# Kernel tuning notes

Hardware: AMD Instinct MI355X
Metric: run time of the kernel (lower is better)

## Reference

```python
import jax, jax.numpy as jnp
import numpy as np

N_NODES = 20000   # batch of nodes (vectorized version of per-node calls)
N_SAMPLE = 32     # num_sample neighbors per node
EMBED_DIM = 256
TABLE_SIZE = 100000


def setup_inputs() -> dict:
    key = jax.random.key(0)
    k1, k2, k3, k4, k5, k6, k7, k8, k9 = jax.random.split(key, 9)
    D = EMBED_DIM
    scale = 1.0 / np.sqrt(D)
    return {
        "node_ids": jax.random.randint(k1, (N_NODES,), 0, TABLE_SIZE),
        "neigh_ids": jax.random.randint(k2, (N_NODES, N_SAMPLE), 0, TABLE_SIZE),
        "feat_table": jax.random.normal(k3, (TABLE_SIZE, D), dtype=jnp.float32),
        "Wq": jax.random.uniform(k4, (D, D), jnp.float32, -scale, scale),
        "bq": jax.random.uniform(k5, (D,), jnp.float32, -scale, scale),
        "Wk": jax.random.uniform(k6, (D, D), jnp.float32, -scale, scale),
        "bk": jax.random.uniform(k7, (D,), jnp.float32, -scale, scale),
        "Wv": jax.random.uniform(k8, (D, D), jnp.float32, -scale, scale),
        "bv": jax.random.uniform(k9, (D,), jnp.float32, -scale, scale),
    }


def reference(node_ids, neigh_ids, feat_table, Wq, bq, Wk, bk, Wv, bv):
    # id2feat lookups
    self_feats = feat_table[node_ids]            # [N, D]
    neigh_feats = feat_table[neigh_ids]          # [N, S, D]
    # context = cat(self, neighbors) along the key/value axis
    ctx = jnp.concatenate([self_feats[:, None, :], neigh_feats], axis=1)  # [N, S+1, D]
    # torch Linear: y = x @ W^T + b
    Q = self_feats @ Wq.T + bq                   # [N, D]
    K = ctx @ Wk.T + bk                          # [N, S+1, D]
    V = ctx @ Wv.T + bv                          # [N, S+1, D]
    scores = jnp.einsum('nd,nkd->nk', Q, K)      # [N, S+1]
    attn = jax.nn.softmax(scores, axis=-1)
    mix = jnp.einsum('nk,nkd->nd', attn, V)      # [N, D]
    out = jnp.tanh(mix)
    # F.normalize(p=2, dim=-1) with eps=1e-12 clamp
    norm = jnp.maximum(jnp.linalg.norm(out, axis=-1, keepdims=True), 1e-12)
    return out / norm
```

## Files before the change

### kernel.cpp

```cpp
#include <hip/hip_runtime.h>
#include <hip/hip_bf16.h>

#define D 256

typedef __bf16 bf16x8 __attribute__((ext_vector_type(8)));
typedef float  f32x4  __attribute__((ext_vector_type(4)));
typedef unsigned short ushort8 __attribute__((ext_vector_type(8)));

static __device__ __forceinline__ unsigned short f2bf_rne(float f) {
    unsigned u = __float_as_uint(f);
    u += 0x7fff + ((u >> 16) & 1);
    return (unsigned short)(u >> 16);
}
static __device__ __forceinline__ float bf2f(unsigned short h) {
    return __uint_as_float(((unsigned)h) << 16);
}
static __device__ __forceinline__ unsigned short f2h(float f) {
    _Float16 h = (_Float16)f;
    unsigned short u; __builtin_memcpy(&u, &h, 2); return u;
}
static __device__ __forceinline__ float h2f(unsigned short u) {
    _Float16 h; __builtin_memcpy(&h, &u, 2); return (float)h;
}

static __device__ __forceinline__ void cp16(const unsigned short* g, unsigned short* l) {
    __builtin_amdgcn_global_load_lds(
        (const __attribute__((address_space(1))) void*)g,
        (__attribute__((address_space(3))) void*)l, 16, 0, 0);
}

static __device__ __forceinline__ void split8(float4 a, float4 b,
                                              ushort8& h, ushort8& l) {
    float v[8] = {a.x, a.y, a.z, a.w, b.x, b.y, b.z, b.w};
    #pragma unroll
    for (int i = 0; i < 8; ++i) {
        unsigned short hh = f2bf_rne(v[i]);
        h[i] = hh;
        l[i] = f2bf_rne(v[i] - bf2f(hh));
    }
}

__global__ __launch_bounds__(256) void convert_w_wstar(
    const float* __restrict__ Wq, const float* __restrict__ Wk,
    const float* __restrict__ Wv, const float* __restrict__ bq,
    unsigned short* __restrict__ wqT_h, unsigned short* __restrict__ wqT_l,
    unsigned short* __restrict__ wkT_h, unsigned short* __restrict__ wkT_l,
    unsigned short* __restrict__ wv_h,  unsigned short* __restrict__ wv_l,
    float* __restrict__ wstar)
{
    if (blockIdx.x == 256) {
        int k = threadIdx.x;
        float s = 0.f;
        for (int n = 0; n < D; ++n) s = fmaf(Wk[n * D + k], bq[n], s);
        wstar[k] = s;
        return;
    }
    int i = blockIdx.x * 256 + threadIdx.x;
    int r = i >> 8, cc = i & 255;
    int ti = cc * D + r;
    float q = Wq[i]; unsigned short qh = f2bf_rne(q);
    wqT_h[ti] = qh; wqT_l[ti] = f2bf_rne(q - bf2f(qh));
    float k = Wk[i]; unsigned short kh = f2bf_rne(k);
    wkT_h[ti] = kh; wkT_l[ti] = f2bf_rne(k - bf2f(kh));
    float v = Wv[i]; unsigned short vh = f2bf_rne(v);
    wv_h[i] = vh; wv_l[i] = f2bf_rne(v - bf2f(vh));
}

__global__ __launch_bounds__(256) void convert_feat_f16_c(
    const float* __restrict__ feat, const float* __restrict__ wstar,
    unsigned short* __restrict__ f16tab, float* __restrict__ c, int T)
{
    const int w = threadIdx.x >> 6, l = threadIdx.x & 63;
    const int row = blockIdx.x * 4 + w;
    if (row >= T) return;
    float4 v = ((const float4*)(feat + (size_t)row * D))[l];
    float4 ws = ((const float4*)wstar)[l];
    ushort4 h;
    h.x = f2h(v.x); h.y = f2h(v.y); h.z = f2h(v.z); h.w = f2h(v.w);
    ((ushort4*)(f16tab + (size_t)row * D))[l] = h;
    float p = v.x * ws.x + v.y * ws.y + v.z * ws.z + v.w * ws.w;
    #pragma unroll
    for (int off = 32; off > 0; off >>= 1) p += __shfl_down(p, off);
    if (l == 0) c[row] = p;
}

template <bool BF16PAIR_OUT, bool AF32>
__global__ __launch_bounds__(256) void mfma_gemm(
    const unsigned short* __restrict__ Ah, const unsigned short* __restrict__ Al,
    const float* __restrict__ Af,
    const int* __restrict__ idx, int M,
    const unsigned short* __restrict__ Bh, const unsigned short* __restrict__ Bl,
    const float* __restrict__ bias,
    float* __restrict__ Cf, unsigned short* __restrict__ Ch,
    unsigned short* __restrict__ Cl, int ldc)
{
    __shared__ __align__(16) unsigned short sAh[128 * 32], sBh[128 * 32];
    __shared__ __align__(16) unsigned short sAl[128 * 32], sBl[128 * 32];

    const int t = threadIdx.x;
    const int w = t >> 6, lane = t & 63;
    const int quad = lane >> 4, mcol = lane & 15;
    const int m0 = blockIdx.x * 128, n0 = blockIdx.y * 128;
    const int wr = (w >> 1) * 64, wc = (w & 1) * 64;

    const int srow = w * 32 + (lane >> 2);
    const int kchunk = (lane & 3) * 8;

    int ar0 = m0 + srow;      if (ar0 > M - 1) ar0 = M - 1;
    int ar1 = m0 + srow + 16; if (ar1 > M - 1) ar1 = M - 1;
    if (idx) { ar0 = idx[ar0]; ar1 = idx[ar1]; }

    const unsigned short *a0h = nullptr, *a1h = nullptr, *a0l = nullptr, *a1l = nullptr;
    const float *af0 = nullptr, *af1 = nullptr;
    if constexpr (AF32) {
        af0 = Af + (size_t)ar0 * D + kchunk;
        af1 = Af + (size_t)ar1 * D + kchunk;
    } else {
        a0h = Ah + (size_t)ar0 * D + kchunk;
        a1h = Ah + (size_t)ar1 * D + kchunk;
        a0l = Al + (size_t)ar0 * D + kchunk;
        a1l = Al + (size_t)ar1 * D + kchunk;
    }
    const unsigned short* b0h = Bh + (size_t)(n0 + srow) * D + kchunk;
    const unsigned short* b1h = Bh + (size_t)(n0 + srow + 16) * D + kchunk;
    const unsigned short* b0l = Bl + (size_t)(n0 + srow) * D + kchunk;
    const unsigned short* b1l = Bl + (size_t)(n0 + srow + 16) * D + kchunk;

    f32x4 acc[4][4];
    #pragma unroll
    for (int i = 0; i < 4; ++i)
        #pragma unroll
        for (int j = 0; j < 4; ++j) acc[i][j] = (f32x4){0.f, 0.f, 0.f, 0.f};

    #pragma unroll
    for (int kb = 0; kb < D; kb += 32) {
        cp16(b0h + kb, &sBh[w * 1024]);
        cp16(b1h + kb, &sBh[w * 1024 + 512]);
        cp16(b0l + kb, &sBl[w * 1024]);
        cp16(b1l + kb, &sBl[w * 1024 + 512]);
        if constexpr (AF32) {
            float4 x0 = *(const float4*)(af0 + kb);
            float4 x1 = *(const float4*)(af0 + kb + 4);
            float4 y0 = *(const float4*)(af1 + kb);
            float4 y1 = *(const float4*)(af1 + kb + 4);
            ushort8 h, l;
            split8(x0, x1, h, l);
            *(ushort8*)&sAh[w * 1024 + lane * 8] = h;
            *(ushort8*)&sAl[w * 1024 + lane * 8] = l;
            split8(y0, y1, h, l);
            *(ushort8*)&sAh[w * 1024 + 512 + lane * 8] = h;
            *(ushort8*)&sAl[w * 1024 + 512 + lane * 8] = l;
        } else {
            cp16(a0h + kb, &sAh[w * 1024]);
            cp16(a1h + kb, &sAh[w * 1024 + 512]);
            cp16(a0l + kb, &sAl[w * 1024]);
            cp16(a1l + kb, &sAl[w * 1024 + 512]);
        }
        __syncthreads();

        bf16x8 fah[4], fbh[4], fal[4], fbl[4];
        #pragma unroll
        for (int i = 0; i < 4; ++i) {
            fah[i] = *(const bf16x8*)&sAh[(wr + i * 16 + mcol) * 32 + quad * 8];
            fbh[i] = *(const bf16x8*)&sBh[(wc + i * 16 + mcol) * 32 + quad * 8];
            fal[i] = *(const bf16x8*)&sAl[(wr + i * 16 + mcol) * 32 + quad * 8];
            fbl[i] = *(const bf16x8*)&sBl[(wc + i * 16 + mcol) * 32 + quad * 8];
        }
        #pragma unroll
        for (int i = 0; i < 4; ++i)
            #pragma unroll
            for (int j = 0; j < 4; ++j) {
                acc[i][j] = __builtin_amdgcn_mfma_f32_16x16x32_bf16(fah[i], fbh[j], acc[i][j], 0, 0, 0);
                acc[i][j] = __builtin_amdgcn_mfma_f32_16x16x32_bf16(fah[i], fbl[j], acc[i][j], 0, 0, 0);
                acc[i][j] = __builtin_amdgcn_mfma_f32_16x16x32_bf16(fal[i], fbh[j], acc[i][j], 0, 0, 0);
            }
        __syncthreads();
    }

    float bb[4];
    #pragma unroll
    for (int j = 0; j < 4; ++j) bb[j] = bias ? bias[n0 + wc + j * 16 + mcol] : 0.f;

    #pragma unroll
    for (int i = 0; i < 4; ++i) {
        #pragma unroll
        for (int r = 0; r < 4; ++r) {
            int m = m0 + wr + i * 16 + quad * 4 + r;
            if (m < M) {
                #pragma unroll
                for (int j = 0; j < 4; ++j) {
                    float v = acc[i][j][r] + bb[j];
                    size_t off = (size_t)m * ldc + n0 + wc + j * 16 + mcol;
                    if constexpr (BF16PAIR_OUT) {
                        unsigned short hh = f2bf_rne(v);
                        Ch[off] = hh;
                        Cl[off] = f2bf_rne(v - bf2f(hh));
                    } else {
                        Cf[off] = v;
                    }
                }
            }
        }
    }
}

template <int S>
__global__ __launch_bounds__(256) void attn_wave(
    const int* __restrict__ node_ids, const int* __restrict__ neigh_ids,
    const float* __restrict__ G, const unsigned short* __restrict__ f16tab,
    const float* __restrict__ c, float* __restrict__ mixf, int N)
{
    constexpr int SP1 = S + 1;
    const int w = threadIdx.x >> 6, l = threadIdx.x & 63;
    const int n = blockIdx.x * 4 + w;
    if (n >= N) return;

    int myid = 0;
    if (l < SP1) myid = (l == 0) ? node_ids[n] : neigh_ids[(size_t)n * S + (l - 1)];
    float myc = (l < SP1) ? c[myid] : 0.f;

    float4 g = ((const float4*)(G + (size_t)n * D))[l];

    ushort4 rows[SP1];
    #pragma unroll
    for (int k = 0; k < SP1; ++k) {
        int idk = __shfl(myid, k);
        rows[k] = ((const ushort4*)(f16tab + (size_t)idk * D))[l];
    }

    float score = -1e30f;
    #pragma unroll
    for (int k = 0; k < SP1; ++k) {
        ushort4 r = rows[k];
        float p = g.x * h2f(r.x) + g.y * h2f(r.y) +
                  g.z * h2f(r.z) + g.w * h2f(r.w);
        #pragma unroll
        for (int off = 1; off < 64; off <<= 1) p += __shfl_xor(p, off);
        if (l == k) score = p + myc;
    }

    float m = score;
    #pragma unroll
    for (int off = 1; off < 64; off <<= 1) m = fmaxf(m, __shfl_xor(m, off));
    float e = (l < SP1) ? __expf(score - m) : 0.f;
    float s = e;
    #pragma unroll
    for (int off = 1; off < 64; off <<= 1) s += __shfl_xor(s, off);
    float attn = e / s;

    float4 mix = {0.f, 0.f, 0.f, 0.f};
    #pragma unroll
    for (int k = 0; k < SP1; ++k) {
        float a = __shfl(attn, k);
        ushort4 r = rows[k];
        mix.x = fmaf(a, h2f(r.x), mix.x);
        mix.y = fmaf(a, h2f(r.y), mix.y);
        mix.z = fmaf(a, h2f(r.z), mix.z);
        mix.w = fmaf(a, h2f(r.w), mix.w);
    }
    ((float4*)(mixf + (size_t)n * D))[l] = mix;
}

__global__ __launch_bounds__(256) void attn_dyn(
    const int* __restrict__ node_ids, const int* __restrict__ neigh_ids,
    const float* __restrict__ G, const unsigned short* __restrict__ f16tab,
    const float* __restrict__ c, float* __restrict__ mixf, int S)
{
    const int n = blockIdx.x, t = threadIdx.x;
    const int w = t >> 6, l = t & 63;
    __shared__ int   ids[128];
    __shared__ float sc[128];
    const int SP1 = S + 1;
    for (int k = t; k < SP1; k += 256)
        ids[k] = (k == 0) ? node_ids[n] : neigh_ids[(size_t)n * S + k - 1];
    __syncthreads();
    float4 g = ((const float4*)(G + (size_t)n * D))[l];
    for (int k = w; k < SP1; k += 4) {
        int id = ids[k];
        ushort4 h4 = ((const ushort4*)(f16tab + (size_t)id * D))[l];
        float p = g.x * h2f(h4.x) + g.y * h2f(h4.y) +
                  g.z * h2f(h4.z) + g.w * h2f(h4.w);
        #pragma unroll
        for (int off = 32; off > 0; off >>= 1) p += __shfl_down(p, off);
        if (l == 0) sc[k] = p + c[id];
    }
    __syncthreads();
    if (t < 64) {
        float v = (t < SP1) ? sc[t] : -1e30f;
        float m = v;
        #pragma unroll
        for (int off = 32; off > 0; off >>= 1) m = fmaxf(m, __shfl_down(m, off));
        m = __shfl(m, 0);
        float e = (t < SP1) ? __expf(v - m) : 0.f;
        float s = e;
        #pragma unroll
        for (int off = 32; off > 0; off >>= 1) s += __shfl_down(s, off);
        s = __shfl(s, 0);
        if (t < SP1) sc[t] = e / s;
    }
    __syncthreads();
    float mix = 0.f;
    for (int k = 0; k < SP1; ++k)
        mix = fmaf(sc[k], h2f(f16tab[(size_t)ids[k] * D + t]), mix);
    mixf[(size_t)n * D + t] = mix;
}

__global__ __launch_bounds__(256) void tanh_norm(
    const float* __restrict__ P, float* __restrict__ out, int N)
{
    const int w = threadIdx.x >> 6, l = threadIdx.x & 63;
    const int row = blockIdx.x * 4 + w;
    if (row >= N) return;
    float4 v = ((const float4*)(P + (size_t)row * D))[l];
    float4 o;
    o.x = tanhf(v.x); o.y = tanhf(v.y); o.z = tanhf(v.z); o.w = tanhf(v.w);
    float ss = o.x * o.x + o.y * o.y + o.z * o.z + o.w * o.w;
    #pragma unroll
    for (int off = 32; off > 0; off >>= 1) ss += __shfl_down(ss, off);
    ss = __shfl(ss, 0);
    float inv = 1.0f / fmaxf(sqrtf(ss), 1e-12f);
    o.x *= inv; o.y *= inv; o.z *= inv; o.w *= inv;
    ((float4*)(out + (size_t)row * D))[l] = o;
}

extern "C" void kernel_launch(void* const* d_in, const int* in_sizes, int n_in,
                              void* d_out, int out_size, void* d_ws, size_t ws_size,
                              hipStream_t stream) {
    const int*   node_ids  = (const int*)  d_in[0];
    const int*   neigh_ids = (const int*)  d_in[1];
    const float* feat      = (const float*)d_in[2];
    const float* Wq        = (const float*)d_in[3];
    const float* bq        = (const float*)d_in[4];
    const float* Wk        = (const float*)d_in[5];
    const float* Wv        = (const float*)d_in[7];
    const float* bv        = (const float*)d_in[8];
    float*       out       = (float*)d_out;

    const int N = in_sizes[0];
    const int S = in_sizes[1] / N;
    const int T = in_sizes[2] / D;

    unsigned short* f16tab = (unsigned short*)d_ws;
    float*          c      = (float*)(f16tab + (size_t)T * D);
    float*          G      = c + T;
    float*          mixf   = G + (size_t)N * D;
    float*          P      = mixf + (size_t)N * D;
    unsigned short* wqT_h  = (unsigned short*)(P + (size_t)N * D);
    unsigned short* wqT_l  = wqT_h + D * D;
    unsigned short* wkT_h  = wqT_l + D * D;
    unsigned short* wkT_l  = wkT_h + D * D;
    unsigned short* wv_h   = wkT_l + D * D;
    unsigned short* wv_l   = wv_h + D * D;
    unsigned short* MT_h   = wv_l + D * D;
    unsigned short* MT_l   = MT_h + D * D;
    float*          wstar  = (float*)(MT_l + D * D);

    convert_w_wstar<<<257, 256, 0, stream>>>(Wq, Wk, Wv, bq,
        wqT_h, wqT_l, wkT_h, wkT_l, wv_h, wv_l, wstar);

    convert_feat_f16_c<<<(T + 3) / 4, 256, 0, stream>>>(feat, wstar, f16tab, c, T);

    {
        dim3 grid(2, 2);
        mfma_gemm<true, false><<<grid, 256, 0, stream>>>(
            wkT_h, wkT_l, nullptr, nullptr, D, wqT_h, wqT_l, nullptr,
            nullptr, MT_h, MT_l, D);
    }
    {
        dim3 grid((N + 127) / 128, 2);
        mfma_gemm<false, true><<<grid, 256, 0, stream>>>(
            nullptr, nullptr, feat, node_ids, N, MT_h, MT_l, nullptr,
            G, nullptr, nullptr, D);
    }
    if (S == 32)
        attn_wave<32><<<(N + 3) / 4, 256, 0, stream>>>(
            node_ids, neigh_ids, G, f16tab, c, mixf, N);
    else
        attn_dyn<<<N, 256, 0, stream>>>(node_ids, neigh_ids, G, f16tab, c, mixf, S);

    {
        dim3 grid((N + 127) / 128, 2);
        mfma_gemm<false, true><<<grid, 256, 0, stream>>>(
            nullptr, nullptr, mixf, nullptr, N, wv_h, wv_l, bv,
            P, nullptr, nullptr, D);
    }
    tanh_norm<<<(N + 3) / 4, 256, 0, stream>>>(P, out, N);
}
```

Measured before the change: 327.1 us.

## Fold key-bias term into G bias, merge convert kernels, shrink GEMM tiles, repack attention

The per-table-row bias dot product c (feat·Wk^T bq) is dropped. Instead wstar is passed as the bias of the G GEMM, so the constant shifts every score equally or is absorbed differently, and the full-table c pass plus its reads are removed. The feature-table fp16 conversion and the weight conversion are merged into one launch. The GEMM tile drops from 128x128 to 64x128 to give more blocks. The attention kernel now has each half-wave process one row with 8-wide fp16 loads, which halves the shuffle reduction depth. Adding wstar to G gives g·x + x·wstar, which equals the old x·(G_old+wstar), so it is mathematically equivalent.

```diff
diff --git a/kernel.cpp b/kernel.cpp
--- a/kernel.cpp
+++ b/kernel.cpp
@@ -5,7 +5,7 @@
 
 typedef __bf16 bf16x8 __attribute__((ext_vector_type(8)));
 typedef float  f32x4  __attribute__((ext_vector_type(4)));
-typedef unsigned short ushort8 __attribute__((ext_vector_type(8)));
+typedef unsigned short ushort8v __attribute__((ext_vector_type(8)));
 
 static __device__ __forceinline__ unsigned short f2bf_rne(float f) {
     unsigned u = __float_as_uint(f);
@@ -30,7 +30,7 @@
 }
 
 static __device__ __forceinline__ void split8(float4 a, float4 b,
-                                              ushort8& h, ushort8& l) {
+                                              ushort8v& h, ushort8v& l) {
     float v[8] = {a.x, a.y, a.z, a.w, b.x, b.y, b.z, b.w};
     #pragma unroll
     for (int i = 0; i < 8; ++i) {
@@ -40,22 +40,36 @@
     }
 }
 
-__global__ __launch_bounds__(256) void convert_w_wstar(
+__global__ __launch_bounds__(256) void convert_all(
+    const float* __restrict__ feat, int T, int nbf,
     const float* __restrict__ Wq, const float* __restrict__ Wk,
     const float* __restrict__ Wv, const float* __restrict__ bq,
+    unsigned short* __restrict__ f16tab,
     unsigned short* __restrict__ wqT_h, unsigned short* __restrict__ wqT_l,
     unsigned short* __restrict__ wkT_h, unsigned short* __restrict__ wkT_l,
     unsigned short* __restrict__ wv_h,  unsigned short* __restrict__ wv_l,
     float* __restrict__ wstar)
 {
-    if (blockIdx.x == 256) {
+    const int bx = blockIdx.x;
+    if (bx < nbf) {
+        const int w = threadIdx.x >> 6, l = threadIdx.x & 63;
+        const int row = bx * 4 + w;
+        if (row >= T) return;
+        float4 v = ((const float4*)(feat + (size_t)row * D))[l];
+        ushort4 h;
+        h.x = f2h(v.x); h.y = f2h(v.y); h.z = f2h(v.z); h.w = f2h(v.w);
+        ((ushort4*)(f16tab + (size_t)row * D))[l] = h;
+        return;
+    }
+    const int wb = bx - nbf;
+    if (wb == 256) {
         int k = threadIdx.x;
         float s = 0.f;
         for (int n = 0; n < D; ++n) s = fmaf(Wk[n * D + k], bq[n], s);
         wstar[k] = s;
         return;
     }
-    int i = blockIdx.x * 256 + threadIdx.x;
+    int i = wb * 256 + threadIdx.x;
     int r = i >> 8, cc = i & 255;
     int ti = cc * D + r;
     float q = Wq[i]; unsigned short qh = f2bf_rne(q);
@@ -66,26 +80,8 @@
     wv_h[i] = vh; wv_l[i] = f2bf_rne(v - bf2f(vh));
 }
 
-__global__ __launch_bounds__(256) void convert_feat_f16_c(
-    const float* __restrict__ feat, const float* __restrict__ wstar,
-    unsigned short* __restrict__ f16tab, float* __restrict__ c, int T)
-{
-    const int w = threadIdx.x >> 6, l = threadIdx.x & 63;
-    const int row = blockIdx.x * 4 + w;
-    if (row >= T) return;
-    float4 v = ((const float4*)(feat + (size_t)row * D))[l];
-    float4 ws = ((const float4*)wstar)[l];
-    ushort4 h;
-    h.x = f2h(v.x); h.y = f2h(v.y); h.z = f2h(v.z); h.w = f2h(v.w);
-    ((ushort4*)(f16tab + (size_t)row * D))[l] = h;
-    float p = v.x * ws.x + v.y * ws.y + v.z * ws.z + v.w * ws.w;
-    #pragma unroll
-    for (int off = 32; off > 0; off >>= 1) p += __shfl_down(p, off);
-    if (l == 0) c[row] = p;
-}
-
 template <bool BF16PAIR_OUT, bool AF32>
-__global__ __launch_bounds__(256) void mfma_gemm(
+__global__ __launch_bounds__(256) void mfma_gemm64(
     const unsigned short* __restrict__ Ah, const unsigned short* __restrict__ Al,
     const float* __restrict__ Af,
     const int* __restrict__ idx, int M,
@@ -94,82 +90,74 @@
     float* __restrict__ Cf, unsigned short* __restrict__ Ch,
     unsigned short* __restrict__ Cl, int ldc)
 {
-    __shared__ __align__(16) unsigned short sAh[128 * 32], sBh[128 * 32];
-    __shared__ __align__(16) unsigned short sAl[128 * 32], sBl[128 * 32];
+    __shared__ __align__(16) unsigned short sAh[64 * 32], sAl[64 * 32];
+    __shared__ __align__(16) unsigned short sBh[128 * 32], sBl[128 * 32];
 
     const int t = threadIdx.x;
     const int w = t >> 6, lane = t & 63;
     const int quad = lane >> 4, mcol = lane & 15;
-    const int m0 = blockIdx.x * 128, n0 = blockIdx.y * 128;
-    const int wr = (w >> 1) * 64, wc = (w & 1) * 64;
-
-    const int srow = w * 32 + (lane >> 2);
-    const int kchunk = (lane & 3) * 8;
-
-    int ar0 = m0 + srow;      if (ar0 > M - 1) ar0 = M - 1;
-    int ar1 = m0 + srow + 16; if (ar1 > M - 1) ar1 = M - 1;
-    if (idx) { ar0 = idx[ar0]; ar1 = idx[ar1]; }
-
-    const unsigned short *a0h = nullptr, *a1h = nullptr, *a0l = nullptr, *a1l = nullptr;
-    const float *af0 = nullptr, *af1 = nullptr;
+    const int m0 = blockIdx.x * 64, n0 = blockIdx.y * 128;
+    const int wc = w * 32;
+
+    const int arow = t >> 2;
+    const int kchunk = (t & 3) * 8;
+
+    int ar = m0 + arow; if (ar > M - 1) ar = M - 1;
+    if (idx) ar = idx[ar];
+
+    const unsigned short *aph = nullptr, *apl = nullptr;
+    const float *apf = nullptr;
     if constexpr (AF32) {
-        af0 = Af + (size_t)ar0 * D + kchunk;
-        af1 = Af + (size_t)ar1 * D + kchunk;
+        apf = Af + (size_t)ar * D + kchunk;
     } else {
-        a0h = Ah + (size_t)ar0 * D + kchunk;
-        a1h = Ah + (size_t)ar1 * D + kchunk;
-        a0l = Al + (size_t)ar0 * D + kchunk;
-        a1l = Al + (size_t)ar1 * D + kchunk;
-    }
-    const unsigned short* b0h = Bh + (size_t)(n0 + srow) * D + kchunk;
-    const unsigned short* b1h = Bh + (size_t)(n0 + srow + 16) * D + kchunk;
-    const unsigned short* b0l = Bl + (size_t)(n0 + srow) * D + kchunk;
-    const unsigned short* b1l = Bl + (size_t)(n0 + srow + 16) * D + kchunk;
-
-    f32x4 acc[4][4];
+        aph = Ah + (size_t)ar * D + kchunk;
+        apl = Al + (size_t)ar * D + kchunk;
+    }
+    const unsigned short* b0h = Bh + (size_t)(n0 + arow) * D + kchunk;
+    const unsigned short* b1h = Bh + (size_t)(n0 + arow + 64) * D + kchunk;
+    const unsigned short* b0l = Bl + (size_t)(n0 + arow) * D + kchunk;
+    const unsigned short* b1l = Bl + (size_t)(n0 + arow + 64) * D + kchunk;
+
+    f32x4 acc[4][2];
     #pragma unroll
     for (int i = 0; i < 4; ++i)
         #pragma unroll
-        for (int j = 0; j < 4; ++j) acc[i][j] = (f32x4){0.f, 0.f, 0.f, 0.f};
+        for (int j = 0; j < 2; ++j) acc[i][j] = (f32x4){0.f, 0.f, 0.f, 0.f};
 
     #pragma unroll
     for (int kb = 0; kb < D; kb += 32) {
-        cp16(b0h + kb, &sBh[w * 1024]);
-        cp16(b1h + kb, &sBh[w * 1024 + 512]);
-        cp16(b0l + kb, &sBl[w * 1024]);
-        cp16(b1l + kb, &sBl[w * 1024 + 512]);
+        cp16(b0h + kb, &sBh[w * 512]);
+        cp16(b1h + kb, &sBh[w * 512 + 2048]);
+        cp16(b0l + kb, &sBl[w * 512]);
+        cp16(b1l + kb, &sBl[w * 512 + 2048]);
         if constexpr (AF32) {
-            float4 x0 = *(const float4*)(af0 + kb);
-            float4 x1 = *(const float4*)(af0 + kb + 4);
-            float4 y0 = *(const float4*)(af1 + kb);
-            float4 y1 = *(const float4*)(af1 + kb + 4);
-            ushort8 h, l;
+            float4 x0 = *(const float4*)(apf + kb);
+            float4 x1 = *(const float4*)(apf + kb + 4);
+            ushort8v h, l;
             split8(x0, x1, h, l);
-            *(ushort8*)&sAh[w * 1024 + lane * 8] = h;
-            *(ushort8*)&sAl[w * 1024 + lane * 8] = l;
-            split8(y0, y1, h, l);
-            *(ushort8*)&sAh[w * 1024 + 512 + lane * 8] = h;
-            *(ushort8*)&sAl[w * 1024 + 512 + lane * 8] = l;
+            *(ushort8v*)&sAh[arow * 32 + kchunk] = h;
+            *(ushort8v*)&sAl[arow * 32 + kchunk] = l;
         } else {
-            cp16(a0h + kb, &sAh[w * 1024]);
-            cp16(a1h + kb, &sAh[w * 1024 + 512]);
-            cp16(a0l + kb, &sAl[w * 1024]);
-            cp16(a1l + kb, &sAl[w * 1024 + 512]);
+            cp16(aph + kb, &sAh[w * 512]);
+            cp16(apl + kb, &sAl[w * 512]);
         }
         __syncthreads();
 
-        bf16x8 fah[4], fbh[4], fal[4], fbl[4];
+        bf16x8 fah[4], fal[4], fbh[2], fbl[2];
         #pragma unroll
         for (int i = 0; i < 4; ++i) {
-            fah[i] = *(const bf16x8*)&sAh[(wr + i * 16 + mcol) * 32 + quad * 8];
-            fbh[i] = *(const bf16x8*)&sBh[(wc + i * 16 + mcol) * 32 + quad * 8];
-            fal[i] = *(const bf16x8*)&sAl[(wr + i * 16 + mcol) * 32 + quad * 8];
-            fbl[i] = *(const bf16x8*)&sBl[(wc + i * 16 + mcol) * 32 + quad * 8];
+            fah[i] = *(const bf16x8*)&sAh[(i * 16 + mcol) * 32 + quad * 8];
+            fal[i] = *(const bf16x8*)&sAl[(i * 16 + mcol) * 32 + quad * 8];
+        }
+        #pragma unroll
+        for (int j = 0; j < 2; ++j) {
+            fbh[j] = *(const bf16x8*)&sBh[(wc + j * 16 + mcol) * 32 + quad * 8];
+            fbl[j] = *(const bf16x8*)&sBl[(wc + j * 16 + mcol) * 32 + quad * 8];
         }
         #pragma unroll
         for (int i = 0; i < 4; ++i)
             #pragma unroll
-            for (int j = 0; j < 4; ++j) {
+            for (int j = 0; j < 2; ++j) {
                 acc[i][j] = __builtin_amdgcn_mfma_f32_16x16x32_bf16(fah[i], fbh[j], acc[i][j], 0, 0, 0);
                 acc[i][j] = __builtin_amdgcn_mfma_f32_16x16x32_bf16(fah[i], fbl[j], acc[i][j], 0, 0, 0);
                 acc[i][j] = __builtin_amdgcn_mfma_f32_16x16x32_bf16(fal[i], fbh[j], acc[i][j], 0, 0, 0);
@@ -177,18 +165,18 @@
         __syncthreads();
     }
 
-    float bb[4];
-    #pragma unroll
-    for (int j = 0; j < 4; ++j) bb[j] = bias ? bias[n0 + wc + j * 16 + mcol] : 0.f;
+    float bb[2];
+    #pragma unroll
+    for (int j = 0; j < 2; ++j) bb[j] = bias ? bias[n0 + wc + j * 16 + mcol] : 0.f;
 
     #pragma unroll
     for (int i = 0; i < 4; ++i) {
         #pragma unroll
         for (int r = 0; r < 4; ++r) {
-            int m = m0 + wr + i * 16 + quad * 4 + r;
+            int m = m0 + i * 16 + quad * 4 + r;
             if (m < M) {
                 #pragma unroll
-                for (int j = 0; j < 4; ++j) {
+                for (int j = 0; j < 2; ++j) {
                     float v = acc[i][j][r] + bb[j];
                     size_t off = (size_t)m * ldc + n0 + wc + j * 16 + mcol;
                     if constexpr (BF16PAIR_OUT) {
@@ -205,66 +193,77 @@
 }
 
 template <int S>
-__global__ __launch_bounds__(256) void attn_wave(
+__global__ __launch_bounds__(256) void attn_wave2(
     const int* __restrict__ node_ids, const int* __restrict__ neigh_ids,
     const float* __restrict__ G, const unsigned short* __restrict__ f16tab,
-    const float* __restrict__ c, float* __restrict__ mixf, int N)
+    float* __restrict__ mixf, int N)
 {
     constexpr int SP1 = S + 1;
+    constexpr int NP  = (SP1 + 1) / 2;
     const int w = threadIdx.x >> 6, l = threadIdx.x & 63;
     const int n = blockIdx.x * 4 + w;
     if (n >= N) return;
 
+    const int h  = l >> 5;
+    const int j  = l & 31;
+
     int myid = 0;
     if (l < SP1) myid = (l == 0) ? node_ids[n] : neigh_ids[(size_t)n * S + (l - 1)];
-    float myc = (l < SP1) ? c[myid] : 0.f;
-
-    float4 g = ((const float4*)(G + (size_t)n * D))[l];
-
-    ushort4 rows[SP1];
-    #pragma unroll
-    for (int k = 0; k < SP1; ++k) {
-        int idk = __shfl(myid, k);
-        rows[k] = ((const ushort4*)(f16tab + (size_t)idk * D))[l];
+
+    float4 g0 = ((const float4*)(G + (size_t)n * D))[j * 2];
+    float4 g1 = ((const float4*)(G + (size_t)n * D))[j * 2 + 1];
+    float gv[8] = {g0.x, g0.y, g0.z, g0.w, g1.x, g1.y, g1.z, g1.w};
+
+    ushort8v rows[NP];
+    #pragma unroll
+    for (int p = 0; p < NP; ++p) {
+        int rix = 2 * p + h; if (rix > SP1 - 1) rix = SP1 - 1;
+        int idk = __shfl(myid, rix);
+        rows[p] = ((const ushort8v*)(f16tab + (size_t)idk * D))[j];
     }
 
     float score = -1e30f;
     #pragma unroll
-    for (int k = 0; k < SP1; ++k) {
-        ushort4 r = rows[k];
-        float p = g.x * h2f(r.x) + g.y * h2f(r.y) +
-                  g.z * h2f(r.z) + g.w * h2f(r.w);
-        #pragma unroll
-        for (int off = 1; off < 64; off <<= 1) p += __shfl_xor(p, off);
-        if (l == k) score = p + myc;
-    }
+    for (int p = 0; p < NP; ++p) {
+        ushort8v r = rows[p];
+        float s = 0.f;
+        #pragma unroll
+        for (int i = 0; i < 8; ++i) s = fmaf(gv[i], h2f(r[i]), s);
+        #pragma unroll
+        for (int off = 1; off < 32; off <<= 1) s += __shfl_xor(s, off);
+        if (j == p) score = s;
+    }
+    const int myrow = 2 * j + h;
+    if (myrow >= SP1) score = -1e30f;
 
     float m = score;
     #pragma unroll
     for (int off = 1; off < 64; off <<= 1) m = fmaxf(m, __shfl_xor(m, off));
-    float e = (l < SP1) ? __expf(score - m) : 0.f;
+    float e = (myrow < SP1) ? __expf(score - m) : 0.f;
     float s = e;
     #pragma unroll
     for (int off = 1; off < 64; off <<= 1) s += __shfl_xor(s, off);
     float attn = e / s;
 
-    float4 mix = {0.f, 0.f, 0.f, 0.f};
-    #pragma unroll
-    for (int k = 0; k < SP1; ++k) {
-        float a = __shfl(attn, k);
-        ushort4 r = rows[k];
-        mix.x = fmaf(a, h2f(r.x), mix.x);
-        mix.y = fmaf(a, h2f(r.y), mix.y);
-        mix.z = fmaf(a, h2f(r.z), mix.z);
-        mix.w = fmaf(a, h2f(r.w), mix.w);
-    }
-    ((float4*)(mixf + (size_t)n * D))[l] = mix;
+    float mix[8] = {0.f, 0.f, 0.f, 0.f, 0.f, 0.f, 0.f, 0.f};
+    #pragma unroll
+    for (int p = 0; p < NP; ++p) {
+        float a = __shfl(attn, p + (l & 32));
+        ushort8v r = rows[p];
+        #pragma unroll
+        for (int i = 0; i < 8; ++i) mix[i] = fmaf(a, h2f(r[i]), mix[i]);
+    }
+    #pragma unroll
+    for (int i = 0; i < 8; ++i) mix[i] += __shfl_xor(mix[i], 32);
+
+    float4 v = {mix[4 * h + 0], mix[4 * h + 1], mix[4 * h + 2], mix[4 * h + 3]};
+    ((float4*)(mixf + (size_t)n * D))[j * 2 + h] = v;
 }
 
 __global__ __launch_bounds__(256) void attn_dyn(
     const int* __restrict__ node_ids, const int* __restrict__ neigh_ids,
     const float* __restrict__ G, const unsigned short* __restrict__ f16tab,
-    const float* __restrict__ c, float* __restrict__ mixf, int S)
+    float* __restrict__ mixf, int S)
 {
     const int n = blockIdx.x, t = threadIdx.x;
     const int w = t >> 6, l = t & 63;
@@ -282,7 +281,7 @@
                   g.z * h2f(h4.z) + g.w * h2f(h4.w);
         #pragma unroll
         for (int off = 32; off > 0; off >>= 1) p += __shfl_down(p, off);
-        if (l == 0) sc[k] = p + c[id];
+        if (l == 0) sc[k] = p;
     }
     __syncthreads();
     if (t < 64) {
@@ -341,8 +340,7 @@
     const int T = in_sizes[2] / D;
 
     unsigned short* f16tab = (unsigned short*)d_ws;
-    float*          c      = (float*)(f16tab + (size_t)T * D);
-    float*          G      = c + T;
+    float*          G      = (float*)(f16tab + (size_t)T * D);
     float*          mixf   = G + (size_t)N * D;
     float*          P      = mixf + (size_t)N * D;
     unsigned short* wqT_h  = (unsigned short*)(P + (size_t)N * D);
@@ -355,32 +353,33 @@
     unsigned short* MT_l   = MT_h + D * D;
     float*          wstar  = (float*)(MT_l + D * D);
 
-    convert_w_wstar<<<257, 256, 0, stream>>>(Wq, Wk, Wv, bq,
+    const int nbf = (T + 3) / 4;
+
+    convert_all<<<nbf + 257, 256, 0, stream>>>(
+        feat, T, nbf, Wq, Wk, Wv, bq, f16tab,
         wqT_h, wqT_l, wkT_h, wkT_l, wv_h, wv_l, wstar);
 
-    convert_feat_f16_c<<<(T + 3) / 4, 256, 0, stream>>>(feat, wstar, f16tab, c, T);
-
     {
-        dim3 grid(2, 2);
-        mfma_gemm<true, false><<<grid, 256, 0, stream>>>(
+        dim3 grid(4, 2);
+        mfma_gemm64<true, false><<<grid, 256, 0, stream>>>(
             wkT_h, wkT_l, nullptr, nullptr, D, wqT_h, wqT_l, nullptr,
             nullptr, MT_h, MT_l, D);
     }
     {
-        dim3 grid((N + 127) / 128, 2);
-        mfma_gemm<false, true><<<grid, 256, 0, stream>>>(
-            nullptr, nullptr, feat, node_ids, N, MT_h, MT_l, nullptr,
+        dim3 grid((N + 63) / 64, 2);
+        mfma_gemm64<false, true><<<grid, 256, 0, stream>>>(
+            nullptr, nullptr, feat, node_ids, N, MT_h, MT_l, wstar,
             G, nullptr, nullptr, D);
     }
     if (S == 32)
-        attn_wave<32><<<(N + 3) / 4, 256, 0, stream>>>(
-            node_ids, neigh_ids, G, f16tab, c, mixf, N);
+        attn_wave2<32><<<(N + 3) / 4, 256, 0, stream>>>(
+            node_ids, neigh_ids, G, f16tab, mixf, N);
     else
-        attn_dyn<<<N, 256, 0, stream>>>(node_ids, neigh_ids, G, f16tab, c, mixf, S);
+        attn_dyn<<<N, 256, 0, stream>>>(node_ids, neigh_ids, G, f16tab, mixf, S);
 
     {
-        dim3 grid((N + 127) / 128, 2);
-        mfma_gemm<false, true><<<grid, 256, 0, stream>>>(
+        dim3 grid((N + 63) / 64, 2);
+        mfma_gemm64<false, true><<<grid, 256, 0, stream>>>(
             nullptr, nullptr, mixf, nullptr, N, wv_h, wv_l, bv,
             P, nullptr, nullptr, D);
     }
```

After: 286.7 us. 1.14x faster.
